# Kernel optimization log

Measured on AMD Instinct MI355X. Metric: run time of the kernel, lower is better.

The kernel has to match this reference:

```python
import jax, jax.numpy as jnp
import numpy as np

B, F, M, C = 4096, 2048, 14, 100
K = 2 ** M  # 16384 latent binary codes


def _codebook(m):
    # itertools.product([0,1], repeat=m) order: row i is binary repr of i, MSB first
    i = jnp.arange(2 ** m)
    j = jnp.arange(m)
    return ((i[:, None] >> (m - 1 - j)[None, :]) & 1).astype(jnp.float32)  # [K, m]


def setup_inputs() -> dict:
    key = jax.random.key(0)
    k1, k2, k3, k4, k5, k6 = jax.random.split(key, 6)
    init_a = 2.0 / np.sqrt(F)
    init_b = 2.0 / np.sqrt(M)
    return {
        "x_in": jax.random.normal(k1, (B, F), dtype=jnp.float32),
        "y_in": jax.random.randint(k2, (B,), 0, C),
        "alpha_0": jax.random.normal(k3, (M,), dtype=jnp.float32),
        "alpha": init_a * jax.random.normal(k4, (M, F), dtype=jnp.float32),
        "beta_0": jax.random.normal(k5, (C,), dtype=jnp.float32),
        "beta": init_b * jax.random.normal(k6, (C, M), dtype=jnp.float32),
    }


def reference(x_in, y_in, alpha_0, alpha, beta_0, beta):
    cb = _codebook(M)  # [K, M]
    # linear_eta
    le = alpha_0[None, :] + x_in @ alpha.T  # [B, M]
    # linear_pi over all codes (mod_codes = 2*cb - 1)
    linear_pi = beta_0[:, None] + beta @ (2.0 * cb - 1.0).T  # [C, K]
    pi = jax.nn.softmax(linear_pi, axis=0)  # exp / sum over classes
    # P(Z|X): exp(cb @ le.T - sum_j softplus(le)) transposed -> [B, K]
    sp = jax.nn.softplus(le)  # log(1 + exp(le)), stable  [B, M]
    P_ZgivenX = jnp.exp((cb @ le.T - jnp.sum(sp, axis=1)[None, :]).T)  # [B, K]
    y1 = jax.nn.one_hot(y_in, C, dtype=le.dtype)  # [B, C]
    numerator = (y1 @ pi) * P_ZgivenX  # [B, K]
    denom = jnp.sum(numerator, axis=1)  # [B]
    # E[Ind Z_j]: masked sum over codes with bit j == 1 == single matmul with cb
    E_IndZ = (numerator @ cb) / denom[:, None]  # [B, M]
    # EI
    EZ = 2.0 * E_IndZ - 1.0
    EI = jnp.sum(y1 * (beta_0[None, :] + EZ @ beta.T))
    # EII
    prob_log = numerator / denom[:, None]
    log_terms = jax.scipy.special.logsumexp(linear_pi, axis=0)  # [K]
    EII = jnp.sum(prob_log * log_terms[None, :])
    # EIII, EIV
    EIII = jnp.sum(E_IndZ * le)
    EIV = jnp.sum(sp)
    return EI - EII + EIII - EIV
```

## Files before the change

kernel.cpp:

```cpp
#include <hip/hip_runtime.h>
#include <math.h>

#define NB 4096
#define NF 2048
#define NM 14
#define NC 100
#define NK 16384

__device__ __forceinline__ float softplus_f(float v) {
    return fmaxf(v, 0.f) + log1pf(__expf(-fabsf(v)));
}

extern "C" __global__ void __launch_bounds__(256) k1_le(
        const float* __restrict__ x, const float* __restrict__ alpha,
        float* __restrict__ le_part) {
    const int tid = threadIdx.x;
    const int wave = tid >> 6, lane = tid & 63;
    const int grp = blockIdx.x >> 1;
    const int half = blockIdx.x & 1;
    const int row0 = grp * 16 + wave * 4;
    const float4* __restrict__ x4 = (const float4*)x;
    const float4* __restrict__ a4 = (const float4*)alpha;
    float acc[4][NM];
#pragma unroll
    for (int r = 0; r < 4; ++r)
#pragma unroll
        for (int j = 0; j < NM; ++j) acc[r][j] = 0.f;
#pragma unroll 1
    for (int cc = 0; cc < 4; ++cc) {
        const int f4i = half * 256 + cc * 64 + lane;
        float4 av[NM];
#pragma unroll
        for (int j = 0; j < NM; ++j) av[j] = a4[j * 512 + f4i];
#pragma unroll
        for (int r = 0; r < 4; ++r) {
            const float4 xv = x4[(row0 + r) * 512 + f4i];
#pragma unroll
            for (int j = 0; j < NM; ++j) {
                acc[r][j] = fmaf(xv.x, av[j].x, acc[r][j]);
                acc[r][j] = fmaf(xv.y, av[j].y, acc[r][j]);
                acc[r][j] = fmaf(xv.z, av[j].z, acc[r][j]);
                acc[r][j] = fmaf(xv.w, av[j].w, acc[r][j]);
            }
        }
    }
#pragma unroll
    for (int m = 1; m < 64; m <<= 1) {
#pragma unroll
        for (int r = 0; r < 4; ++r)
#pragma unroll
            for (int j = 0; j < NM; ++j)
                acc[r][j] += __shfl_xor(acc[r][j], m, 64);
    }
    if (lane == 0) {
        float* dst = le_part + half * (NB * NM) + row0 * NM;
#pragma unroll
        for (int r = 0; r < 4; ++r)
#pragma unroll
            for (int j = 0; j < NM; ++j)
                dst[r * NM + j] = acc[r][j];
    }
}

extern "C" __global__ void __launch_bounds__(256) k2_sl(
        const float* __restrict__ beta, const float* __restrict__ beta0,
        float2* __restrict__ SL) {
    __shared__ float b2[NC * NM];
    __shared__ float base_s[NC];
    __shared__ float Sp[4][64];
    const int tid = threadIdx.x;
    for (int i = tid; i < NC * NM; i += 256) b2[i] = 2.f * beta[i];
    if (tid < NC) {
        float s = beta0[tid];
        for (int j = 0; j < NM; ++j) s -= beta[tid * NM + j];
        base_s[tid] = s;
    }
    __syncthreads();
    const int kl = tid & 63, q = tid >> 6;
    const int k = blockIdx.x * 64 + kl;
    float bits[NM];
#pragma unroll
    for (int j = 0; j < NM; ++j) bits[j] = (float)((k >> (13 - j)) & 1);
    float S = 0.f;
    for (int c = q * 25; c < q * 25 + 25; ++c) {
        float d = base_s[c];
#pragma unroll
        for (int j = 0; j < NM; ++j) d = fmaf(bits[j], b2[c * NM + j], d);
        S += __expf(d);
    }
    Sp[q][kl] = S;
    __syncthreads();
    if (tid < 64) {
        const float Sf = Sp[0][tid] + Sp[1][tid] + Sp[2][tid] + Sp[3][tid];
        SL[blockIdx.x * 64 + tid] = make_float2(1.f / Sf, __logf(Sf));
    }
}

extern "C" __global__ void __launch_bounds__(256) k3_main(
        const float* __restrict__ le_part, const float* __restrict__ alpha0,
        const int* __restrict__ y, const float* __restrict__ beta,
        const float* __restrict__ beta0, const float2* __restrict__ SL,
        float* __restrict__ partial) {
    __shared__ float t_s[8][16];
    __shared__ float sp_s[8][16];
    __shared__ float cs_s[8];
    __shared__ float f_s[8];
    __shared__ float Alds[128][8];
    __shared__ float Elds[128][8];
    __shared__ float red[4][16];
    const int tid = threadIdx.x;
    const int b0 = blockIdx.x * 8;

    if (tid < 128) {
        const int r = tid >> 4, j = tid & 15;
        if (j < NM) {
            const int yv = y[b0 + r];
            const float lv = le_part[(b0 + r) * NM + j]
                           + le_part[NB * NM + (b0 + r) * NM + j] + alpha0[j];
            t_s[r][j] = lv + 2.f * beta[yv * NM + j];
            sp_s[r][j] = softplus_f(lv);
        }
    }
    __syncthreads();
    if (tid < 8) {
        const int yv = y[b0 + tid];
        float cs = beta0[yv];
        for (int j = 0; j < NM; ++j) {
            cs -= beta[yv * NM + j];
            cs += fmaxf(t_s[tid][j], 0.f) - sp_s[tid][j];
        }
        cs_s[tid] = cs;
    }
#pragma unroll
    for (int e = 0; e < 4; ++e) {
        const int idx = tid + 256 * e;
        const int r = idx & 7, h = idx >> 3;
        float A = 0.f, ub = 0.f;
#pragma unroll
        for (int j = 0; j < 7; ++j) {
            const float tv = t_s[r][j];
            A += ((h >> (6 - j)) & 1) ? tv : 0.f;
            ub += fmaxf(tv, 0.f);
        }
        const float Ap = A - ub;
        Alds[h][r] = Ap;
        Elds[h][r] = __expf(Ap);
    }
    const int l = tid & 127;
    float eb[8], aterm[8];
#pragma unroll
    for (int r = 0; r < 8; ++r) {
        float A = 0.f, ub = 0.f;
#pragma unroll
        for (int j = 7; j < NM; ++j) {
            const float tv = t_s[r][j];
            A += ((l >> (13 - j)) & 1) ? tv : 0.f;
            ub += fmaxf(tv, 0.f);
        }
        aterm[r] = A - ub;
        eb[r] = __expf(A - ub);
    }
    __syncthreads();

    float U[8], V[8];
#pragma unroll
    for (int r = 0; r < 8; ++r) { U[r] = 0.f; V[r] = 0.f; }
    const int c = tid >> 7;
#pragma unroll 4
    for (int i = 0; i < 64; ++i) {
        const float2 sl = SL[i * 256 + tid];
        const int h = 2 * i + c;
        const float4 Aa = *(const float4*)&Alds[h][0];
        const float4 Ab = *(const float4*)&Alds[h][4];
        const float4 Ea = *(const float4*)&Elds[h][0];
        const float4 Eb = *(const float4*)&Elds[h][4];
        const float Ar[8] = {Aa.x, Aa.y, Aa.z, Aa.w, Ab.x, Ab.y, Ab.z, Ab.w};
        const float Er[8] = {Ea.x, Ea.y, Ea.z, Ea.w, Eb.x, Eb.y, Eb.z, Eb.w};
#pragma unroll
        for (int r = 0; r < 8; ++r) {
            const float rest = Er[r] * sl.x;
            U[r] += rest;
            V[r] = fmaf(rest, Ar[r] - sl.y, V[r]);
        }
    }
    float vals[16];
#pragma unroll
    for (int r = 0; r < 8; ++r) {
        vals[r] = eb[r] * U[r];
        vals[8 + r] = eb[r] * fmaf(aterm[r], U[r], V[r]);
    }
#pragma unroll
    for (int m = 1; m < 64; m <<= 1)
#pragma unroll
        for (int q2 = 0; q2 < 16; ++q2)
            vals[q2] += __shfl_xor(vals[q2], m, 64);
    const int wv = tid >> 6, lane = tid & 63;
    if (lane == 0) {
#pragma unroll
        for (int q2 = 0; q2 < 16; ++q2) red[wv][q2] = vals[q2];
    }
    __syncthreads();
    if (tid < 16)
        red[0][tid] = red[0][tid] + red[1][tid] + red[2][tid] + red[3][tid];
    __syncthreads();
    if (tid < 8)
        f_s[tid] = cs_s[tid] + red[0][8 + tid] / red[0][tid];
    __syncthreads();
    if (tid == 0) {
        float s = 0.f;
#pragma unroll
        for (int r = 0; r < 8; ++r) s += f_s[r];
        partial[blockIdx.x] = s;
    }
}

extern "C" __global__ void __launch_bounds__(256) k4_reduce(
        const float* __restrict__ partial, float* __restrict__ out) {
    __shared__ float red[4];
    const int tid = threadIdx.x;
    float s = partial[tid] + partial[tid + 256];
#pragma unroll
    for (int m = 1; m < 64; m <<= 1) s += __shfl_xor(s, m, 64);
    const int wv = tid >> 6, lane = tid & 63;
    if (lane == 0) red[wv] = s;
    __syncthreads();
    if (tid == 0) out[0] = red[0] + red[1] + red[2] + red[3];
}

extern "C" void kernel_launch(void* const* d_in, const int* in_sizes, int n_in,
                              void* d_out, int out_size, void* d_ws, size_t ws_size,
                              hipStream_t stream) {
    const float* x      = (const float*)d_in[0];
    const int*   y      = (const int*)d_in[1];
    const float* alpha0 = (const float*)d_in[2];
    const float* alpha  = (const float*)d_in[3];
    const float* beta0  = (const float*)d_in[4];
    const float* beta   = (const float*)d_in[5];

    char* ws = (char*)d_ws;
    float*  le_part = (float*)ws;
    float2* SL      = (float2*)(ws + 2 * NB * NM * 4);
    float*  partial = (float*)(ws + 2 * NB * NM * 4 + NK * 8);
    float*  out     = (float*)d_out;

    k1_le<<<512, 256, 0, stream>>>(x, alpha, le_part);
    k2_sl<<<256, 256, 0, stream>>>(beta, beta0, SL);
    k3_main<<<512, 256, 0, stream>>>(le_part, alpha0, y, beta, beta0, SL, partial);
    k4_reduce<<<1, 256, 0, stream>>>(partial, out);
}
```

Measured before the change: 121.7 us.

## Merge le and SL kernels, fold final reduce into main via last-block atomic

```diff
diff --git a/kernel.cpp b/kernel.cpp
--- a/kernel.cpp
+++ b/kernel.cpp
@@ -11,88 +11,89 @@
     return fmaxf(v, 0.f) + log1pf(__expf(-fabsf(v)));
 }
 
-extern "C" __global__ void __launch_bounds__(256) k1_le(
+extern "C" __global__ void __launch_bounds__(256) kA(
         const float* __restrict__ x, const float* __restrict__ alpha,
-        float* __restrict__ le_part) {
+        float* __restrict__ le_part,
+        const float* __restrict__ beta, const float* __restrict__ beta0,
+        float2* __restrict__ SL, unsigned int* __restrict__ cnt) {
     const int tid = threadIdx.x;
-    const int wave = tid >> 6, lane = tid & 63;
-    const int grp = blockIdx.x >> 1;
-    const int half = blockIdx.x & 1;
-    const int row0 = grp * 16 + wave * 4;
-    const float4* __restrict__ x4 = (const float4*)x;
-    const float4* __restrict__ a4 = (const float4*)alpha;
-    float acc[4][NM];
-#pragma unroll
-    for (int r = 0; r < 4; ++r)
-#pragma unroll
-        for (int j = 0; j < NM; ++j) acc[r][j] = 0.f;
+    if (blockIdx.x < 512) {
+        const int wave = tid >> 6, lane = tid & 63;
+        const int grp = (int)blockIdx.x >> 1;
+        const int half = blockIdx.x & 1;
+        const int row0 = grp * 16 + wave * 4;
+        const float4* __restrict__ x4 = (const float4*)x;
+        const float4* __restrict__ a4 = (const float4*)alpha;
+        float acc[4][NM];
+#pragma unroll
+        for (int r = 0; r < 4; ++r)
+#pragma unroll
+            for (int j = 0; j < NM; ++j) acc[r][j] = 0.f;
 #pragma unroll 1
-    for (int cc = 0; cc < 4; ++cc) {
-        const int f4i = half * 256 + cc * 64 + lane;
-        float4 av[NM];
-#pragma unroll
-        for (int j = 0; j < NM; ++j) av[j] = a4[j * 512 + f4i];
-#pragma unroll
-        for (int r = 0; r < 4; ++r) {
-            const float4 xv = x4[(row0 + r) * 512 + f4i];
-#pragma unroll
-            for (int j = 0; j < NM; ++j) {
-                acc[r][j] = fmaf(xv.x, av[j].x, acc[r][j]);
-                acc[r][j] = fmaf(xv.y, av[j].y, acc[r][j]);
-                acc[r][j] = fmaf(xv.z, av[j].z, acc[r][j]);
-                acc[r][j] = fmaf(xv.w, av[j].w, acc[r][j]);
+        for (int cc = 0; cc < 4; ++cc) {
+            const int f4i = half * 256 + cc * 64 + lane;
+            float4 av[NM];
+#pragma unroll
+            for (int j = 0; j < NM; ++j) av[j] = a4[j * 512 + f4i];
+#pragma unroll
+            for (int r = 0; r < 4; ++r) {
+                const float4 xv = x4[(row0 + r) * 512 + f4i];
+#pragma unroll
+                for (int j = 0; j < NM; ++j) {
+                    acc[r][j] = fmaf(xv.x, av[j].x, acc[r][j]);
+                    acc[r][j] = fmaf(xv.y, av[j].y, acc[r][j]);
+                    acc[r][j] = fmaf(xv.z, av[j].z, acc[r][j]);
+                    acc[r][j] = fmaf(xv.w, av[j].w, acc[r][j]);
+                }
             }
         }
-    }
-#pragma unroll
-    for (int m = 1; m < 64; m <<= 1) {
-#pragma unroll
-        for (int r = 0; r < 4; ++r)
-#pragma unroll
-            for (int j = 0; j < NM; ++j)
-                acc[r][j] += __shfl_xor(acc[r][j], m, 64);
-    }
-    if (lane == 0) {
-        float* dst = le_part + half * (NB * NM) + row0 * NM;
-#pragma unroll
-        for (int r = 0; r < 4; ++r)
-#pragma unroll
-            for (int j = 0; j < NM; ++j)
-                dst[r * NM + j] = acc[r][j];
-    }
-}
-
-extern "C" __global__ void __launch_bounds__(256) k2_sl(
-        const float* __restrict__ beta, const float* __restrict__ beta0,
-        float2* __restrict__ SL) {
-    __shared__ float b2[NC * NM];
-    __shared__ float base_s[NC];
-    __shared__ float Sp[4][64];
-    const int tid = threadIdx.x;
-    for (int i = tid; i < NC * NM; i += 256) b2[i] = 2.f * beta[i];
-    if (tid < NC) {
-        float s = beta0[tid];
-        for (int j = 0; j < NM; ++j) s -= beta[tid * NM + j];
-        base_s[tid] = s;
-    }
-    __syncthreads();
-    const int kl = tid & 63, q = tid >> 6;
-    const int k = blockIdx.x * 64 + kl;
-    float bits[NM];
-#pragma unroll
-    for (int j = 0; j < NM; ++j) bits[j] = (float)((k >> (13 - j)) & 1);
-    float S = 0.f;
-    for (int c = q * 25; c < q * 25 + 25; ++c) {
-        float d = base_s[c];
-#pragma unroll
-        for (int j = 0; j < NM; ++j) d = fmaf(bits[j], b2[c * NM + j], d);
-        S += __expf(d);
-    }
-    Sp[q][kl] = S;
-    __syncthreads();
-    if (tid < 64) {
-        const float Sf = Sp[0][tid] + Sp[1][tid] + Sp[2][tid] + Sp[3][tid];
-        SL[blockIdx.x * 64 + tid] = make_float2(1.f / Sf, __logf(Sf));
+#pragma unroll
+        for (int m = 1; m < 64; m <<= 1) {
+#pragma unroll
+            for (int r = 0; r < 4; ++r)
+#pragma unroll
+                for (int j = 0; j < NM; ++j)
+                    acc[r][j] += __shfl_xor(acc[r][j], m, 64);
+        }
+        if (lane == 0) {
+            float* dst = le_part + half * (NB * NM) + row0 * NM;
+#pragma unroll
+            for (int r = 0; r < 4; ++r)
+#pragma unroll
+                for (int j = 0; j < NM; ++j)
+                    dst[r * NM + j] = acc[r][j];
+        }
+    } else {
+        __shared__ float b2[NC * NM];
+        __shared__ float base_s[NC];
+        __shared__ float Sp[4][64];
+        const int kb = (int)blockIdx.x - 512;
+        if (kb == 0 && tid == 0) *cnt = 0u;
+        for (int i = tid; i < NC * NM; i += 256) b2[i] = 2.f * beta[i];
+        if (tid < NC) {
+            float s = beta0[tid];
+            for (int j = 0; j < NM; ++j) s -= beta[tid * NM + j];
+            base_s[tid] = s;
+        }
+        __syncthreads();
+        const int kl = tid & 63, q = tid >> 6;
+        const int k = kb * 64 + kl;
+        float bits[NM];
+#pragma unroll
+        for (int j = 0; j < NM; ++j) bits[j] = (float)((k >> (13 - j)) & 1);
+        float S = 0.f;
+        for (int c = q * 25; c < q * 25 + 25; ++c) {
+            float d = base_s[c];
+#pragma unroll
+            for (int j = 0; j < NM; ++j) d = fmaf(bits[j], b2[c * NM + j], d);
+            S += __expf(d);
+        }
+        Sp[q][kl] = S;
+        __syncthreads();
+        if (tid < 64) {
+            const float Sf = Sp[0][tid] + Sp[1][tid] + Sp[2][tid] + Sp[3][tid];
+            SL[kb * 64 + tid] = make_float2(1.f / Sf, __logf(Sf));
+        }
     }
 }
 
@@ -100,14 +101,16 @@
         const float* __restrict__ le_part, const float* __restrict__ alpha0,
         const int* __restrict__ y, const float* __restrict__ beta,
         const float* __restrict__ beta0, const float2* __restrict__ SL,
-        float* __restrict__ partial) {
+        float* __restrict__ partial, unsigned int* __restrict__ cnt,
+        float* __restrict__ out) {
     __shared__ float t_s[8][16];
     __shared__ float sp_s[8][16];
     __shared__ float cs_s[8];
     __shared__ float f_s[8];
-    __shared__ float Alds[128][8];
+    __shared__ float EAlds[128][8];
     __shared__ float Elds[128][8];
     __shared__ float red[4][16];
+    __shared__ unsigned last_s;
     const int tid = threadIdx.x;
     const int b0 = blockIdx.x * 8;
 
@@ -143,8 +146,9 @@
             ub += fmaxf(tv, 0.f);
         }
         const float Ap = A - ub;
-        Alds[h][r] = Ap;
-        Elds[h][r] = __expf(Ap);
+        const float E = __expf(Ap);
+        Elds[h][r] = E;
+        EAlds[h][r] = E * Ap;
     }
     const int l = tid & 127;
     float eb[8], aterm[8];
@@ -169,18 +173,20 @@
 #pragma unroll 4
     for (int i = 0; i < 64; ++i) {
         const float2 sl = SL[i * 256 + tid];
+        const float xw = sl.x;
+        const float zw = sl.x * sl.y;
         const int h = 2 * i + c;
-        const float4 Aa = *(const float4*)&Alds[h][0];
-        const float4 Ab = *(const float4*)&Alds[h][4];
+        const float4 Pa = *(const float4*)&EAlds[h][0];
+        const float4 Pb = *(const float4*)&EAlds[h][4];
         const float4 Ea = *(const float4*)&Elds[h][0];
         const float4 Eb = *(const float4*)&Elds[h][4];
-        const float Ar[8] = {Aa.x, Aa.y, Aa.z, Aa.w, Ab.x, Ab.y, Ab.z, Ab.w};
+        const float Pr[8] = {Pa.x, Pa.y, Pa.z, Pa.w, Pb.x, Pb.y, Pb.z, Pb.w};
         const float Er[8] = {Ea.x, Ea.y, Ea.z, Ea.w, Eb.x, Eb.y, Eb.z, Eb.w};
 #pragma unroll
         for (int r = 0; r < 8; ++r) {
-            const float rest = Er[r] * sl.x;
-            U[r] += rest;
-            V[r] = fmaf(rest, Ar[r] - sl.y, V[r]);
+            U[r] = fmaf(Er[r], xw, U[r]);
+            V[r] = fmaf(Pr[r], xw, V[r]);
+            V[r] = fmaf(Er[r], -zw, V[r]);
         }
     }
     float vals[16];
@@ -210,21 +216,24 @@
         float s = 0.f;
 #pragma unroll
         for (int r = 0; r < 8; ++r) s += f_s[r];
-        partial[blockIdx.x] = s;
-    }
-}
-
-extern "C" __global__ void __launch_bounds__(256) k4_reduce(
-        const float* __restrict__ partial, float* __restrict__ out) {
-    __shared__ float red[4];
-    const int tid = threadIdx.x;
-    float s = partial[tid] + partial[tid + 256];
-#pragma unroll
-    for (int m = 1; m < 64; m <<= 1) s += __shfl_xor(s, m, 64);
-    const int wv = tid >> 6, lane = tid & 63;
-    if (lane == 0) red[wv] = s;
-    __syncthreads();
-    if (tid == 0) out[0] = red[0] + red[1] + red[2] + red[3];
+        __hip_atomic_store(&partial[blockIdx.x], s, __ATOMIC_RELEASE,
+                           __HIP_MEMORY_SCOPE_AGENT);
+        const unsigned old = __hip_atomic_fetch_add(cnt, 1u, __ATOMIC_ACQ_REL,
+                                                    __HIP_MEMORY_SCOPE_AGENT);
+        last_s = (old == 511u) ? 1u : 0u;
+    }
+    __syncthreads();
+    if (last_s) {
+        float s = __hip_atomic_load(&partial[tid], __ATOMIC_RELAXED,
+                                    __HIP_MEMORY_SCOPE_AGENT)
+                + __hip_atomic_load(&partial[tid + 256], __ATOMIC_RELAXED,
+                                    __HIP_MEMORY_SCOPE_AGENT);
+#pragma unroll
+        for (int m = 1; m < 64; m <<= 1) s += __shfl_xor(s, m, 64);
+        if (lane == 0) red[0][wv] = s;
+        __syncthreads();
+        if (tid == 0) out[0] = red[0][0] + red[0][1] + red[0][2] + red[0][3];
+    }
 }
 
 extern "C" void kernel_launch(void* const* d_in, const int* in_sizes, int n_in,
@@ -238,13 +247,13 @@
     const float* beta   = (const float*)d_in[5];
 
     char* ws = (char*)d_ws;
-    float*  le_part = (float*)ws;
-    float2* SL      = (float2*)(ws + 2 * NB * NM * 4);
-    float*  partial = (float*)(ws + 2 * NB * NM * 4 + NK * 8);
-    float*  out     = (float*)d_out;
-
-    k1_le<<<512, 256, 0, stream>>>(x, alpha, le_part);
-    k2_sl<<<256, 256, 0, stream>>>(beta, beta0, SL);
-    k3_main<<<512, 256, 0, stream>>>(le_part, alpha0, y, beta, beta0, SL, partial);
-    k4_reduce<<<1, 256, 0, stream>>>(partial, out);
-}
+    float*        le_part = (float*)ws;
+    float2*       SL      = (float2*)(ws + 2 * NB * NM * 4);
+    float*        partial = (float*)(ws + 2 * NB * NM * 4 + NK * 8);
+    unsigned int* cnt     = (unsigned int*)(ws + 2 * NB * NM * 4 + NK * 8 + 512 * 4);
+    float*        out     = (float*)d_out;
+
+    kA<<<768, 256, 0, stream>>>(x, alpha, le_part, beta, beta0, SL, cnt);
+    k3_main<<<512, 256, 0, stream>>>(le_part, alpha0, y, beta, beta0, SL,
+                                     partial, cnt, out);
+}
```

After: 117.0 us. 1.04x faster.
